# Optimization experiments

Hardware: AMD Instinct MI355X
Metric: run time of the kernel (lower is better)

Reference implementation:

```python
import jax, jax.numpy as jnp
import numpy as np

N = 10000        # num_nodes
E = 160000       # num_edges (before self loops)
D_IN = 256       # input_dim
H = 128          # hidden_dim (= per-head out_channels)
HEADS = 4
HD = HEADS * H   # 512
L = 16           # num_layers
OUT = 1024       # output_dim
G = 8            # num graphs in batch
EPS = 1e-5


def _layer_norm(x, w, b):
    m = jnp.mean(x, axis=-1, keepdims=True)
    v = jnp.mean(jnp.square(x - m), axis=-1, keepdims=True)
    return (x - m) / jnp.sqrt(v + EPS) * w + b


def setup_inputs() -> dict:
    key = jax.random.key(0)
    ks = jax.random.split(key, 20)
    s = 0.05
    x = jax.random.normal(ks[0], (N, D_IN), jnp.float32)
    edge_index = jax.random.randint(ks[1], (2, E), 0, N, dtype=jnp.int64)
    batch = jnp.sort(jax.random.randint(ks[2], (N,), 0, G, dtype=jnp.int64))
    return {
        "x": x,
        "edge_index": edge_index,
        "batch": batch,
        "W_in": jax.random.normal(ks[3], (D_IN, H), jnp.float32) * s,
        "b_in": jnp.zeros((H,), jnp.float32),
        "ln_in_w": jnp.ones((H,), jnp.float32),
        "ln_in_b": jnp.zeros((H,), jnp.float32),
        "Wsrc": jax.random.normal(ks[4], (L, H, HD), jnp.float32) * s,
        "Wdst": jax.random.normal(ks[5], (L, H, HD), jnp.float32) * s,
        "att_src": jax.random.normal(ks[6], (L, HEADS, H), jnp.float32) * s,
        "att_dst": jax.random.normal(ks[7], (L, HEADS, H), jnp.float32) * s,
        "Wout": jax.random.normal(ks[8], (L, HD, H), jnp.float32) * s,
        "bout": jnp.zeros((L, H), jnp.float32),
        "ln_w": jnp.ones((L, H), jnp.float32),
        "ln_b": jnp.zeros((L, H), jnp.float32),
        "Wp1": jax.random.normal(ks[9], (H, OUT), jnp.float32) * s,
        "bp1": jnp.zeros((OUT,), jnp.float32),
        "Wp2": jax.random.normal(ks[10], (OUT, OUT), jnp.float32) * s,
        "bp2": jnp.zeros((OUT,), jnp.float32),
    }


def reference(x, edge_index, batch, W_in, b_in, ln_in_w, ln_in_b,
              Wsrc, Wdst, att_src, att_dst, Wout, bout, ln_w, ln_b,
              Wp1, bp1, Wp2, bp2):
    # add self loops once (same edge set every layer)
    loop = jnp.arange(N, dtype=edge_index.dtype)
    e_src = jnp.concatenate([edge_index[0], loop])  # x_j (source)
    e_dst = jnp.concatenate([edge_index[1], loop])  # x_i (target / aggregate index)

    h = jax.nn.relu(_layer_norm(x @ W_in + b_in, ln_in_w, ln_in_b))  # [N, H]

    for l in range(L):
        hs = (h[e_src] @ Wsrc[l]).reshape(-1, HEADS, H)  # [E2, heads, H]
        hd = (h[e_dst] @ Wdst[l]).reshape(-1, HEADS, H)
        a = jnp.sum(hs * att_src[l], axis=-1) + jnp.sum(hd * att_dst[l], axis=-1)  # [E2, heads]
        a = jax.nn.leaky_relu(a, 0.2)
        # NOTE: faithful to source -- softmax over HEADS per edge, not over neighbors
        a = jax.nn.softmax(a, axis=-1)
        msg = (hs * a[..., None]).reshape(-1, HD)  # [E2, HD]
        agg = jax.ops.segment_sum(msg, e_dst, num_segments=N)  # [N, HD]
        out = agg @ Wout[l] + bout[l]
        h = jax.nn.relu(_layer_norm(out + h, ln_w[l], ln_b[l]))  # residual: H == H

    g = jax.ops.segment_max(h, batch, num_segments=G)  # global max pool [G, H]
    g = jax.nn.relu(g @ Wp1 + bp1)
    return g @ Wp2 + bp2  # [G, OUT]
```

## Files before the change

kernel.cpp:

```cpp
#include <hip/hip_runtime.h>
#include <hip/hip_bf16.h>

#define N_NODES 10000
#define E_EDGES 160000
#define E2 (E_EDGES + N_NODES)
#define D_IN 256
#define H 128
#define HEADS 4
#define HD 512
#define L_LAYERS 16
#define OUT_DIM 1024
#define G_GRAPHS 8
#define EPS 1e-5f
#define SPAD 10016

typedef unsigned short ushort_t;
typedef __attribute__((ext_vector_type(8))) short short8;
typedef __attribute__((ext_vector_type(4))) float f32x4;
typedef __attribute__((ext_vector_type(4))) unsigned u32x4;

__device__ __forceinline__ f32x4 mfma16(short8 a, short8 b, f32x4 c) {
    return __builtin_amdgcn_mfma_f32_16x16x32_bf16(a, b, c, 0, 0, 0);
}
__device__ __forceinline__ unsigned short f2b(float f) {
    unsigned u = __float_as_uint(f);
    u += 0x7fffu + ((u >> 16) & 1u);
    return (unsigned short)(u >> 16);
}
__device__ __forceinline__ float b2f(unsigned short b) {
    return __uint_as_float((unsigned)b << 16);
}
__device__ __forceinline__ unsigned pk2(float lo, float hi) {
    __hip_bfloat162 p = __float22bfloat162_rn(make_float2(lo, hi));
    return *(unsigned*)&p;
}

__global__ void k_zero(int* deg, int* cur, unsigned* g) {
    int i = blockIdx.x * blockDim.x + threadIdx.x;
    if (i < N_NODES) { deg[i] = 0; cur[i] = 0; }
    if (i < G_GRAPHS * H) g[i] = 0u;
}

__global__ void k_count(const int* ei, int* deg) {
    int e = blockIdx.x * blockDim.x + threadIdx.x;
    if (e >= E2) return;
    int d = (e < E_EDGES) ? ei[E_EDGES + e] : (e - E_EDGES);
    atomicAdd(&deg[d], 1);
}

__global__ void k_scan(const int* deg, int* rs) {
    __shared__ int s[1024];
    int t = threadIdx.x;
    int base = t * 10;
    int loc[10], run = 0;
    #pragma unroll
    for (int i = 0; i < 10; i++) {
        int idx = base + i;
        int v = (idx < N_NODES) ? deg[idx] : 0;
        loc[i] = run; run += v;
    }
    s[t] = run;
    __syncthreads();
    for (int off = 1; off < 1024; off <<= 1) {
        int xv = (t >= off) ? s[t - off] : 0;
        __syncthreads();
        s[t] += xv;
        __syncthreads();
    }
    int excl = s[t] - run;
    #pragma unroll
    for (int i = 0; i < 10; i++) {
        int idx = base + i;
        if (idx <= N_NODES) rs[idx] = excl + loc[i];
    }
}

__global__ void k_fill(const int* ei, const int* rs, int* cur, int* elist) {
    int e = blockIdx.x * blockDim.x + threadIdx.x;
    if (e >= E2) return;
    int s, d;
    if (e < E_EDGES) { s = ei[e]; d = ei[E_EDGES + e]; }
    else { s = d = e - E_EDGES; }
    int pos = atomicAdd(&cur[d], 1);
    elist[rs[d] + pos] = s;
}

__global__ void k_vw(const float* Wsrc, const float* Wdst,
                     const float* att_src, const float* att_dst,
                     float* vsrc, float* vdst) {
    int l = blockIdx.x;
    int t = threadIdx.x;
    int head = t >> 7, j = t & 127;
    const float* Ws = Wsrc + (size_t)l * H * HD;
    const float* Wd = Wdst + (size_t)l * H * HD;
    const float* As = att_src + (size_t)l * HEADS * H;
    const float* Ad = att_dst + (size_t)l * HEADS * H;
    float ss = 0.f, sd = 0.f;
    for (int k = 0; k < H; k++) {
        ss += Ws[(size_t)j * HD + head * H + k] * As[head * H + k];
        sd += Wd[(size_t)j * HD + head * H + k] * Ad[head * H + k];
    }
    vsrc[(size_t)l * HD + head * H + j] = ss;
    vdst[(size_t)l * HD + head * H + j] = sd;
}

__global__ __launch_bounds__(256) void k_mm(const float* __restrict__ Wsrc,
        const float* __restrict__ Wout, float* __restrict__ M) {
    __shared__ float As[32][33];
    __shared__ float Bs[32][128];
    int bid = blockIdx.x;
    int q = bid & 3, hh = (bid >> 2) & 3, l = bid >> 4;
    int t = threadIdx.x;
    int ty = t >> 4, tx = t & 15;
    const float* WsB = Wsrc + (size_t)l * H * HD + (size_t)hh * 128;
    const float* WoB = Wout + (size_t)l * HD * H + (size_t)hh * 128 * H;
    float acc[2][8];
    #pragma unroll
    for (int r = 0; r < 2; r++)
        #pragma unroll
        for (int c = 0; c < 8; c++) acc[r][c] = 0.f;
    for (int kt = 0; kt < 4; kt++) {
        #pragma unroll
        for (int i = 0; i < 4; i++) {
            int lin = i * 256 + t;
            int rr = lin >> 5, cc = lin & 31;
            As[rr][cc] = WsB[(size_t)(q * 32 + rr) * HD + kt * 32 + cc];
        }
        #pragma unroll
        for (int i = 0; i < 16; i++) {
            int lin = i * 256 + t;
            int rr = lin >> 7, cc = lin & 127;
            Bs[rr][cc] = WoB[(size_t)(kt * 32 + rr) * H + cc];
        }
        __syncthreads();
        #pragma unroll
        for (int kk = 0; kk < 32; kk++) {
            float a0 = As[ty * 2][kk], a1 = As[ty * 2 + 1][kk];
            float4 b0 = *(const float4*)&Bs[kk][tx * 8];
            float4 b1 = *(const float4*)&Bs[kk][tx * 8 + 4];
            acc[0][0] += a0 * b0.x; acc[0][1] += a0 * b0.y;
            acc[0][2] += a0 * b0.z; acc[0][3] += a0 * b0.w;
            acc[0][4] += a0 * b1.x; acc[0][5] += a0 * b1.y;
            acc[0][6] += a0 * b1.z; acc[0][7] += a0 * b1.w;
            acc[1][0] += a1 * b0.x; acc[1][1] += a1 * b0.y;
            acc[1][2] += a1 * b0.z; acc[1][3] += a1 * b0.w;
            acc[1][4] += a1 * b1.x; acc[1][5] += a1 * b1.y;
            acc[1][6] += a1 * b1.z; acc[1][7] += a1 * b1.w;
        }
        __syncthreads();
    }
    #pragma unroll
    for (int r = 0; r < 2; r++)
        #pragma unroll
        for (int c = 0; c < 8; c++)
            M[(size_t)l * HD * H + (size_t)(hh * 128 + q * 32 + ty * 2 + r) * H + tx * 8 + c]
                = acc[r][c];
}

__global__ void k_pack_out2(const float* M, ushort_t* Wh, ushort_t* Wl) {
    int idx = blockIdx.x * 256 + threadIdx.x;
    int l = idx >> 16, rem = idx & 65535;
    int k = rem >> 7, col = rem & 127;
    float v = M[(size_t)l * HD * H + (size_t)k * H + col];
    unsigned short hi = f2b(v);
    unsigned short lo = f2b(v - b2f(hi));
    int nt = col >> 4, ks = k >> 5, lhi = (k >> 3) & 3, llo = col & 15, j = k & 7;
    size_t addr = (size_t)l * 65536 + (((size_t)(nt * 16 + ks) * 64) + lhi * 16 + llo) * 8 + j;
    Wh[addr] = hi;
    Wl[addr] = lo;
}

__global__ void k_pack_win(const float* W, ushort_t* Wp) {
    int idx = blockIdx.x * 256 + threadIdx.x;
    int k = idx >> 7, col = idx & 127;
    float v = W[(size_t)k * H + col];
    int nt = col >> 4, ks = k >> 5, lhi = (k >> 3) & 3, llo = col & 15, j = k & 7;
    Wp[(((size_t)(nt * 8 + ks) * 64) + lhi * 16 + llo) * 8 + j] = f2b(v);
}

__global__ __launch_bounds__(256) void k_in_mfma(
        const float* __restrict__ x, const ushort_t* __restrict__ WpI,
        const float* __restrict__ b_in, const float* __restrict__ lnw,
        const float* __restrict__ lnb, const float* __restrict__ vs,
        const float* __restrict__ vd, float* __restrict__ as0, float* __restrict__ ad0,
        float* __restrict__ h, ushort_t* __restrict__ hb) {
    __shared__ float part1[4][16], part2[4][16];
    __shared__ float apart[4][8][16];
    int t = threadIdx.x, w = t >> 6, lane = t & 63;
    int row0 = blockIdx.x * 16;
    int ar = lane & 15, ac = (lane >> 4) * 8;
    short8 a[8];
    #pragma unroll
    for (int ks = 0; ks < 8; ks++) {
        const float* xp = x + (size_t)(row0 + ar) * D_IN + ks * 32 + ac;
        float4 xa = *(const float4*)xp;
        float4 xb = *(const float4*)(xp + 4);
        u32x4 u;
        u.x = pk2(xa.x, xa.y); u.y = pk2(xa.z, xa.w);
        u.z = pk2(xb.x, xb.y); u.w = pk2(xb.z, xb.w);
        a[ks] = *(short8*)&u;
    }
    const ushort_t* B0 = WpI + ((size_t)(w * 2 + 0) * 8) * 64 * 8;
    const ushort_t* B1 = WpI + ((size_t)(w * 2 + 1) * 8) * 64 * 8;
    f32x4 c0 = {0.f, 0.f, 0.f, 0.f}, c1 = {0.f, 0.f, 0.f, 0.f};
    #pragma unroll
    for (int ks = 0; ks < 8; ks++) {
        short8 b0 = *(const short8*)(B0 + ((size_t)ks * 64 + lane) * 8);
        short8 b1 = *(const short8*)(B1 + ((size_t)ks * 64 + lane) * 8);
        c0 = mfma16(a[ks], b0, c0);
        c1 = mfma16(a[ks], b1, c1);
    }
    int col0 = w * 32 + ar, col1 = w * 32 + 16 + ar;
    int rb = (lane >> 4) * 4;
    float v0[4], v1[4], y0[4], y1[4];
    #pragma unroll
    for (int r = 0; r < 4; r++) {
        v0[r] = c0[r] + b_in[col0];
        v1[r] = c1[r] + b_in[col1];
        float p1 = v0[r] + v1[r];
        float p2 = v0[r] * v0[r] + v1[r] * v1[r];
        #pragma unroll
        for (int off = 1; off < 16; off <<= 1) {
            p1 += __shfl_xor(p1, off);
            p2 += __shfl_xor(p2, off);
        }
        if (ar == 0) { part1[w][rb + r] = p1; part2[w][rb + r] = p2; }
    }
    __syncthreads();
    #pragma unroll
    for (int r = 0; r < 4; r++) {
        int lr = rb + r;
        int row = row0 + lr;
        float s1 = part1[0][lr] + part1[1][lr] + part1[2][lr] + part1[3][lr];
        float s2 = part2[0][lr] + part2[1][lr] + part2[2][lr] + part2[3][lr];
        float m = s1 * (1.f / 128.f);
        float var = s2 * (1.f / 128.f) - m * m;
        float is = rsqrtf(var + EPS);
        y0[r] = fmaxf((v0[r] - m) * is * lnw[col0] + lnb[col0], 0.f);
        y1[r] = fmaxf((v1[r] - m) * is * lnw[col1] + lnb[col1], 0.f);
        h[(size_t)row * H + col0] = y0[r];
        h[(size_t)row * H + col1] = y1[r];
        hb[(size_t)row * H + col0] = f2b(y0[r]);
        hb[(size_t)row * H + col1] = f2b(y1[r]);
    }
    #pragma unroll
    for (int comp = 0; comp < 8; comp++) {
        float vc0 = (comp < 4) ? vs[comp * H + col0] : vd[(comp - 4) * H + col0];
        float vc1 = (comp < 4) ? vs[comp * H + col1] : vd[(comp - 4) * H + col1];
        float p[4];
        #pragma unroll
        for (int r = 0; r < 4; r++) p[r] = y0[r] * vc0 + y1[r] * vc1;
        #pragma unroll
        for (int off = 1; off < 16; off <<= 1)
            #pragma unroll
            for (int r = 0; r < 4; r++) p[r] += __shfl_xor(p[r], off);
        if (ar == 0)
            #pragma unroll
            for (int r = 0; r < 4; r++) apart[w][comp][rb + r] = p[r];
    }
    __syncthreads();
    if (t < 128) {
        int lr = t >> 3, comp = t & 7;
        float s = apart[0][comp][lr] + apart[1][comp][lr]
                + apart[2][comp][lr] + apart[3][comp][lr];
        int node = row0 + lr;
        if (comp < 4) as0[node * 4 + comp] = s;
        else          ad0[node * 4 + comp - 4] = s;
    }
}

#define CONS(uv, wt) do { \
    float f0 = __uint_as_float((uv).x << 16); \
    float f1 = __uint_as_float((uv).x & 0xffff0000u); \
    float f2 = __uint_as_float((uv).y << 16); \
    float f3 = __uint_as_float((uv).y & 0xffff0000u); \
    float f4 = __uint_as_float((uv).z << 16); \
    float f5 = __uint_as_float((uv).z & 0xffff0000u); \
    float f6 = __uint_as_float((uv).w << 16); \
    float f7 = __uint_as_float((uv).w & 0xffff0000u); \
    acc0[0] += (wt).x * f0; acc0[1] += (wt).x * f1; acc0[2] += (wt).x * f2; acc0[3] += (wt).x * f3; \
    acc0[4] += (wt).x * f4; acc0[5] += (wt).x * f5; acc0[6] += (wt).x * f6; acc0[7] += (wt).x * f7; \
    acc1[0] += (wt).y * f0; acc1[1] += (wt).y * f1; acc1[2] += (wt).y * f2; acc1[3] += (wt).y * f3; \
    acc1[4] += (wt).y * f4; acc1[5] += (wt).y * f5; acc1[6] += (wt).y * f6; acc1[7] += (wt).y * f7; \
    acc2[0] += (wt).z * f0; acc2[1] += (wt).z * f1; acc2[2] += (wt).z * f2; acc2[3] += (wt).z * f3; \
    acc2[4] += (wt).z * f4; acc2[5] += (wt).z * f5; acc2[6] += (wt).z * f6; acc2[7] += (wt).z * f7; \
    acc3[0] += (wt).w * f0; acc3[1] += (wt).w * f1; acc3[2] += (wt).w * f2; acc3[3] += (wt).w * f3; \
    acc3[4] += (wt).w * f4; acc3[5] += (wt).w * f5; acc3[6] += (wt).w * f6; acc3[7] += (wt).w * f7; \
} while (0)

__global__ __launch_bounds__(256) void k_gather(
        const ushort_t* __restrict__ hb, const float4* __restrict__ as4,
        const float4* __restrict__ ad4, const int* __restrict__ rs,
        const int* __restrict__ elist, ushort_t* __restrict__ T) {
    __shared__ int sl[4][64];
    __shared__ float wl[4][64][4];
    int t = threadIdx.x, w = t >> 6, lane = t & 63;
    int node = blockIdx.x * 4 + w;
    int start = rs[node], end = rs[node + 1];
    int g = lane >> 4, i = lane & 15;
    const char* hbc = (const char*)hb;
    unsigned ibyte = (unsigned)(i << 4);
    float acc0[8], acc1[8], acc2[8], acc3[8];
    #pragma unroll
    for (int c = 0; c < 8; c++) { acc0[c] = 0.f; acc1[c] = 0.f; acc2[c] = 0.f; acc3[c] = 0.f; }
    for (int c0 = start; c0 < end; c0 += 64) {
        int cnt = min(64, end - c0);
        if (lane < cnt) {
            int s = elist[c0 + lane];
            sl[w][lane] = s;
            float4 adv = ad4[node];
            float4 av = as4[s];
            float l0 = av.x + adv.x, l1 = av.y + adv.y, l2 = av.z + adv.z, l3 = av.w + adv.w;
            l0 = (l0 > 0.f) ? l0 : 0.2f * l0;
            l1 = (l1 > 0.f) ? l1 : 0.2f * l1;
            l2 = (l2 > 0.f) ? l2 : 0.2f * l2;
            l3 = (l3 > 0.f) ? l3 : 0.2f * l3;
            float mx = fmaxf(fmaxf(l0, l1), fmaxf(l2, l3));
            float e0 = expf(l0 - mx), e1 = expf(l1 - mx), e2 = expf(l2 - mx), e3 = expf(l3 - mx);
            float inv = 1.f / (e0 + e1 + e2 + e3);
            wl[w][lane][0] = e0 * inv;
            wl[w][lane][1] = e1 * inv;
            wl[w][lane][2] = e2 * inv;
            wl[w][lane][3] = e3 * inv;
        } else {
            sl[w][lane] = 0;
            wl[w][lane][0] = 0.f; wl[w][lane][1] = 0.f;
            wl[w][lane][2] = 0.f; wl[w][lane][3] = 0.f;
        }
        __asm__ volatile("s_waitcnt lgkmcnt(0)" ::: "memory");
        int rounds = (cnt + 15) >> 4;
        for (int jj = 0; jj < rounds; jj++) {
            int j = (jj << 4) + g;
            unsigned o0 = ((unsigned)sl[w][j]      << 8) + ibyte;
            unsigned o1 = ((unsigned)sl[w][j + 4]  << 8) + ibyte;
            unsigned o2 = ((unsigned)sl[w][j + 8]  << 8) + ibyte;
            unsigned o3 = ((unsigned)sl[w][j + 12] << 8) + ibyte;
            u32x4 v0 = *(const u32x4*)(hbc + o0);
            u32x4 v1 = *(const u32x4*)(hbc + o1);
            u32x4 v2 = *(const u32x4*)(hbc + o2);
            u32x4 v3 = *(const u32x4*)(hbc + o3);
            { float4 wt = *(const float4*)wl[w][j];      CONS(v0, wt); }
            { float4 wt = *(const float4*)wl[w][j + 4];  CONS(v1, wt); }
            { float4 wt = *(const float4*)wl[w][j + 8];  CONS(v2, wt); }
            { float4 wt = *(const float4*)wl[w][j + 12]; CONS(v3, wt); }
        }
    }
    float out[8];
    #pragma unroll
    for (int c = 0; c < 8; c++) {
        float v0 = acc0[c], v1 = acc1[c], v2 = acc2[c], v3 = acc3[c];
        v0 += __shfl_xor(v0, 16); v0 += __shfl_xor(v0, 32);
        v1 += __shfl_xor(v1, 16); v1 += __shfl_xor(v1, 32);
        v2 += __shfl_xor(v2, 16); v2 += __shfl_xor(v2, 32);
        v3 += __shfl_xor(v3, 16); v3 += __shfl_xor(v3, 32);
        out[c] = (g == 0) ? v0 : ((g == 1) ? v1 : ((g == 2) ? v2 : v3));
    }
    u32x4 o;
    o.x = pk2(out[0], out[1]);
    o.y = pk2(out[2], out[3]);
    o.z = pk2(out[4], out[5]);
    o.w = pk2(out[6], out[7]);
    *(u32x4*)(T + (size_t)node * HD + g * 128 + i * 8) = o;
}

__global__ __launch_bounds__(256) void k_post(
        const ushort_t* __restrict__ T, const ushort_t* __restrict__ Wh,
        const ushort_t* __restrict__ Wl, const float* __restrict__ bout,
        const float* __restrict__ lnw, const float* __restrict__ lnb,
        const float* __restrict__ vsn, const float* __restrict__ vdn,
        float* __restrict__ asn, float* __restrict__ adn, int doAlpha,
        float* __restrict__ h, ushort_t* __restrict__ hbo, int l) {
    __shared__ ushort_t frag[1024 * 8];
    __shared__ float part1[4][16], part2[4][16];
    __shared__ float apart[4][8][16];
    int t = threadIdx.x, w = t >> 6, lane = t & 63;
    int row0 = blockIdx.x * 16;
    #pragma unroll
    for (int ii = 0; ii < 4; ii++) {
        int c = ii * 256 + t;
        int row = c >> 6, ks = (c >> 2) & 15, sub = c & 3;
        u32x4 v = *(const u32x4*)(T + (size_t)(row0 + row) * HD + ks * 32 + sub * 8);
        int gidx = (sub * 16 + row) * 16 + (ks ^ row);
        *(u32x4*)((char*)frag + gidx * 16) = v;
    }
    __syncthreads();
    int ar = lane & 15;
    short8 a[16];
    #pragma unroll
    for (int ks = 0; ks < 16; ks++)
        a[ks] = *(const short8*)((const char*)frag + (lane * 16 + (ks ^ ar)) * 16);
    const ushort_t* WLh = Wh + (size_t)l * 65536;
    const ushort_t* WLl = Wl + (size_t)l * 65536;
    f32x4 c0 = {0.f, 0.f, 0.f, 0.f}, c1 = {0.f, 0.f, 0.f, 0.f};
    #pragma unroll
    for (int ks = 0; ks < 16; ks++) {
        short8 b0 = *(const short8*)(WLh + ((size_t)((w * 2 + 0) * 16 + ks) * 64 + lane) * 8);
        short8 b1 = *(const short8*)(WLh + ((size_t)((w * 2 + 1) * 16 + ks) * 64 + lane) * 8);
        c0 = mfma16(a[ks], b0, c0);
        c1 = mfma16(a[ks], b1, c1);
    }
    #pragma unroll
    for (int ks = 0; ks < 16; ks++) {
        short8 b0 = *(const short8*)(WLl + ((size_t)((w * 2 + 0) * 16 + ks) * 64 + lane) * 8);
        short8 b1 = *(const short8*)(WLl + ((size_t)((w * 2 + 1) * 16 + ks) * 64 + lane) * 8);
        c0 = mfma16(a[ks], b0, c0);
        c1 = mfma16(a[ks], b1, c1);
    }
    const float* bo = bout + (size_t)l * H;
    const float* gw = lnw + (size_t)l * H;
    const float* gb = lnb + (size_t)l * H;
    int col0 = w * 32 + ar, col1 = w * 32 + 16 + ar;
    int rb = (lane >> 4) * 4;
    float v0[4], v1[4], y0[4], y1[4];
    #pragma unroll
    for (int r = 0; r < 4; r++) {
        int row = row0 + rb + r;
        v0[r] = c0[r] + bo[col0] + h[(size_t)row * H + col0];
        v1[r] = c1[r] + bo[col1] + h[(size_t)row * H + col1];
        float p1 = v0[r] + v1[r];
        float p2 = v0[r] * v0[r] + v1[r] * v1[r];
        #pragma unroll
        for (int off = 1; off < 16; off <<= 1) {
            p1 += __shfl_xor(p1, off);
            p2 += __shfl_xor(p2, off);
        }
        if (ar == 0) { part1[w][rb + r] = p1; part2[w][rb + r] = p2; }
    }
    __syncthreads();
    #pragma unroll
    for (int r = 0; r < 4; r++) {
        int lr = rb + r;
        int row = row0 + lr;
        float s1 = part1[0][lr] + part1[1][lr] + part1[2][lr] + part1[3][lr];
        float s2 = part2[0][lr] + part2[1][lr] + part2[2][lr] + part2[3][lr];
        float m = s1 * (1.f / 128.f);
        float var = s2 * (1.f / 128.f) - m * m;
        float is = rsqrtf(var + EPS);
        y0[r] = fmaxf((v0[r] - m) * is * gw[col0] + gb[col0], 0.f);
        y1[r] = fmaxf((v1[r] - m) * is * gw[col1] + gb[col1], 0.f);
        h[(size_t)row * H + col0] = y0[r];
        h[(size_t)row * H + col1] = y1[r];
        hbo[(size_t)row * H + col0] = f2b(y0[r]);
        hbo[(size_t)row * H + col1] = f2b(y1[r]);
    }
    if (doAlpha) {
        #pragma unroll
        for (int comp = 0; comp < 8; comp++) {
            float vc0 = (comp < 4) ? vsn[comp * H + col0] : vdn[(comp - 4) * H + col0];
            float vc1 = (comp < 4) ? vsn[comp * H + col1] : vdn[(comp - 4) * H + col1];
            float p[4];
            #pragma unroll
            for (int r = 0; r < 4; r++) p[r] = y0[r] * vc0 + y1[r] * vc1;
            #pragma unroll
            for (int off = 1; off < 16; off <<= 1)
                #pragma unroll
                for (int r = 0; r < 4; r++) p[r] += __shfl_xor(p[r], off);
            if (ar == 0)
                #pragma unroll
                for (int r = 0; r < 4; r++) apart[w][comp][rb + r] = p[r];
        }
        __syncthreads();
        if (t < 128) {
            int lr = t >> 3, comp = t & 7;
            float s = apart[0][comp][lr] + apart[1][comp][lr]
                    + apart[2][comp][lr] + apart[3][comp][lr];
            int node = row0 + lr;
            if (comp < 4) asn[node * 4 + comp] = s;
            else          adn[node * 4 + comp - 4] = s;
        }
    }
}

__global__ void k_pool(const float* __restrict__ h, const int* __restrict__ batch,
                       unsigned* __restrict__ g) {
    __shared__ float lm[G_GRAPHS][H];
    int t = threadIdx.x;
    #pragma unroll
    for (int i = 0; i < G_GRAPHS; i++) lm[i][t] = 0.f;
    int n0 = blockIdx.x * 100, n1 = n0 + 100;
    for (int n = n0; n < n1; n++) {
        int b = batch[n];
        lm[b][t] = fmaxf(lm[b][t], h[(size_t)n * H + t]);
    }
    #pragma unroll
    for (int i = 0; i < G_GRAPHS; i++)
        atomicMax(&g[i * H + t], __float_as_uint(lm[i][t]));
}

__global__ void k_mlp1(const unsigned* __restrict__ g, const float* __restrict__ Wp1,
                       const float* __restrict__ bp1, float* __restrict__ g1) {
    __shared__ float gs[H];
    int gr = blockIdx.x >> 2, ch = blockIdx.x & 3;
    int t = threadIdx.x;
    if (t < H) gs[t] = __uint_as_float(g[gr * H + t]);
    __syncthreads();
    int col = ch * 256 + t;
    float acc = 0.f;
    for (int k = 0; k < H; k++) acc += gs[k] * Wp1[(size_t)k * OUT_DIM + col];
    acc += bp1[col];
    g1[(size_t)gr * OUT_DIM + col] = fmaxf(acc, 0.f);
}

__global__ void k_mlp2(const float* __restrict__ g1, const float* __restrict__ Wp2,
                       const float* __restrict__ bp2, float* __restrict__ out) {
    __shared__ float gs[OUT_DIM];
    __shared__ float part[4][64];
    int gr = blockIdx.x >> 4, ch = blockIdx.x & 15;
    int t = threadIdx.x;
    int ci = t & 63, si = t >> 6;
    for (int i = t; i < OUT_DIM; i += 256) gs[i] = g1[(size_t)gr * OUT_DIM + i];
    __syncthreads();
    int col = ch * 64 + ci;
    float acc = 0.f;
    for (int k = si * 256; k < si * 256 + 256; k++)
        acc += gs[k] * Wp2[(size_t)k * OUT_DIM + col];
    part[si][ci] = acc;
    __syncthreads();
    if (si == 0) {
        float r = part[0][ci] + part[1][ci] + part[2][ci] + part[3][ci] + bp2[col];
        out[(size_t)gr * OUT_DIM + col] = r;
    }
}

extern "C" void kernel_launch(void* const* d_in, const int* in_sizes, int n_in,
                              void* d_out, int out_size, void* d_ws, size_t ws_size,
                              hipStream_t stream) {
    const float* x       = (const float*)d_in[0];
    const int*   ei      = (const int*)d_in[1];
    const int*   batch   = (const int*)d_in[2];
    const float* W_in    = (const float*)d_in[3];
    const float* b_in    = (const float*)d_in[4];
    const float* ln_in_w = (const float*)d_in[5];
    const float* ln_in_b = (const float*)d_in[6];
    const float* Wsrc    = (const float*)d_in[7];
    const float* Wdst    = (const float*)d_in[8];
    const float* att_src = (const float*)d_in[9];
    const float* att_dst = (const float*)d_in[10];
    const float* Wout    = (const float*)d_in[11];
    const float* bout    = (const float*)d_in[12];
    const float* ln_w    = (const float*)d_in[13];
    const float* ln_b    = (const float*)d_in[14];
    const float* Wp1     = (const float*)d_in[15];
    const float* bp1     = (const float*)d_in[16];
    const float* Wp2     = (const float*)d_in[17];
    const float* bp2     = (const float*)d_in[18];

    char* w = (char*)d_ws;
    auto alloc = [&](size_t bytes) { void* p = w; w += (bytes + 255) & ~(size_t)255; return p; };
    float*     h     = (float*)alloc((size_t)N_NODES * H * 4);
    ushort_t*  hb0   = (ushort_t*)alloc((size_t)SPAD * H * 2);
    ushort_t*  hb1   = (ushort_t*)alloc((size_t)SPAD * H * 2);
    ushort_t*  T     = (ushort_t*)alloc((size_t)SPAD * HD * 2);
    float*     as0   = (float*)alloc((size_t)SPAD * HEADS * 4);
    float*     ad0   = (float*)alloc((size_t)SPAD * HEADS * 4);
    float*     as1   = (float*)alloc((size_t)SPAD * HEADS * 4);
    float*     ad1   = (float*)alloc((size_t)SPAD * HEADS * 4);
    float*     vsrc  = (float*)alloc((size_t)L_LAYERS * HD * 4);
    float*     vdst  = (float*)alloc((size_t)L_LAYERS * HD * 4);
    float*     M     = (float*)alloc((size_t)L_LAYERS * HD * H * 4);
    ushort_t*  WpH   = (ushort_t*)alloc((size_t)L_LAYERS * 65536 * 2);
    ushort_t*  WpL   = (ushort_t*)alloc((size_t)L_LAYERS * 65536 * 2);
    ushort_t*  WpI   = (ushort_t*)alloc((size_t)D_IN * H * 2);
    int*       deg   = (int*)alloc((size_t)N_NODES * 4);
    int*       rs    = (int*)alloc((size_t)(N_NODES + 1) * 4);
    int*       cur   = (int*)alloc((size_t)N_NODES * 4);
    int*       elist = (int*)alloc((size_t)E2 * 4);
    unsigned*  g     = (unsigned*)alloc((size_t)G_GRAPHS * H * 4);
    float*     g1    = (float*)alloc((size_t)G_GRAPHS * OUT_DIM * 4);

    k_zero<<<40, 256, 0, stream>>>(deg, cur, g);
    k_count<<<(E2 + 255) / 256, 256, 0, stream>>>(ei, deg);
    k_scan<<<1, 1024, 0, stream>>>(deg, rs);
    k_fill<<<(E2 + 255) / 256, 256, 0, stream>>>(ei, rs, cur, elist);
    k_vw<<<L_LAYERS, 512, 0, stream>>>(Wsrc, Wdst, att_src, att_dst, vsrc, vdst);
    k_mm<<<256, 256, 0, stream>>>(Wsrc, Wout, M);
    k_pack_out2<<<4096, 256, 0, stream>>>(M, WpH, WpL);
    k_pack_win<<<128, 256, 0, stream>>>(W_in, WpI);
    k_in_mfma<<<N_NODES / 16, 256, 0, stream>>>(x, WpI, b_in, ln_in_w, ln_in_b,
                                                vsrc, vdst, as0, ad0, h, hb0);

    for (int l = 0; l < L_LAYERS; l++) {
        const ushort_t* hbi = (l & 1) ? hb1 : hb0;
        ushort_t*       hbo = (l & 1) ? hb0 : hb1;
        const float* aA = (l & 1) ? as1 : as0;
        const float* dA = (l & 1) ? ad1 : ad0;
        float* aB = (l & 1) ? as0 : as1;
        float* dB = (l & 1) ? ad0 : ad1;
        int ln = (l + 1 < L_LAYERS) ? (l + 1) : (L_LAYERS - 1);
        k_gather<<<N_NODES / 4, 256, 0, stream>>>(hbi, (const float4*)aA, (const float4*)dA,
                                                  rs, elist, T);
        k_post<<<N_NODES / 16, 256, 0, stream>>>(
            T, WpH, WpL, bout, ln_w, ln_b,
            vsrc + (size_t)ln * HD, vdst + (size_t)ln * HD,
            aB, dB, (l + 1 < L_LAYERS) ? 1 : 0, h, hbo, l);
    }

    k_pool<<<100, 128, 0, stream>>>(h, batch, g);
    k_mlp1<<<G_GRAPHS * 4, 256, 0, stream>>>(g, Wp1, bp1, g1);
    k_mlp2<<<G_GRAPHS * 16, 256, 0, stream>>>(g1, Wp2, bp2, (float*)d_out);
}
```

Before: 728.6 us.

## Parallelize attention-vector precompute, add nontemporal hints, trim gather tail loop

The per-layer attention-vector kernel is rewritten so that each wavefront reduces one output with a shuffle reduction, replacing the old layout of 16 blocks with a serial 128-step loop per thread and strided loads. Streaming buffers (h, the T intermediate) now use nontemporal loads and stores so they bypass cache retention. The gather loop now processes neighbors in 4-wide steps for the remainder instead of padding to a multiple of 16. Nontemporal hints could hurt if these buffers benefit from L2/MALL reuse between kernels.

```diff
diff --git a/kernel.cpp b/kernel.cpp
--- a/kernel.cpp
+++ b/kernel.cpp
@@ -85,23 +85,29 @@
     elist[rs[d] + pos] = s;
 }
 
-__global__ void k_vw(const float* Wsrc, const float* Wdst,
-                     const float* att_src, const float* att_dst,
-                     float* vsrc, float* vdst) {
-    int l = blockIdx.x;
-    int t = threadIdx.x;
-    int head = t >> 7, j = t & 127;
-    const float* Ws = Wsrc + (size_t)l * H * HD;
-    const float* Wd = Wdst + (size_t)l * H * HD;
-    const float* As = att_src + (size_t)l * HEADS * H;
-    const float* Ad = att_dst + (size_t)l * HEADS * H;
-    float ss = 0.f, sd = 0.f;
-    for (int k = 0; k < H; k++) {
-        ss += Ws[(size_t)j * HD + head * H + k] * As[head * H + k];
-        sd += Wd[(size_t)j * HD + head * H + k] * Ad[head * H + k];
-    }
-    vsrc[(size_t)l * HD + head * H + j] = ss;
-    vdst[(size_t)l * HD + head * H + j] = sd;
+__global__ __launch_bounds__(256) void k_vw(const float* __restrict__ Wsrc,
+        const float* __restrict__ Wdst, const float* __restrict__ att_src,
+        const float* __restrict__ att_dst, float* __restrict__ vsrc,
+        float* __restrict__ vdst) {
+    int t = threadIdx.x, w = t >> 6, lane = t & 63;
+    int unit = blockIdx.x * 4 + w;
+    int j = unit & 127, head = (unit >> 7) & 3, l = unit >> 9;
+    int k2 = lane * 2;
+    const float2 ws = *(const float2*)(Wsrc + (size_t)l * H * HD + (size_t)j * HD + head * 128 + k2);
+    const float2 wd = *(const float2*)(Wdst + (size_t)l * H * HD + (size_t)j * HD + head * 128 + k2);
+    const float2 as = *(const float2*)(att_src + (size_t)l * HEADS * H + head * 128 + k2);
+    const float2 ad = *(const float2*)(att_dst + (size_t)l * HEADS * H + head * 128 + k2);
+    float p = ws.x * as.x + ws.y * as.y;
+    float q = wd.x * ad.x + wd.y * ad.y;
+    #pragma unroll
+    for (int off = 32; off > 0; off >>= 1) {
+        p += __shfl_down(p, off);
+        q += __shfl_down(q, off);
+    }
+    if (lane == 0) {
+        vsrc[(size_t)l * HD + head * H + j] = p;
+        vdst[(size_t)l * HD + head * H + j] = q;
+    }
 }
 
 __global__ __launch_bounds__(256) void k_mm(const float* __restrict__ Wsrc,
@@ -238,8 +244,8 @@
         float is = rsqrtf(var + EPS);
         y0[r] = fmaxf((v0[r] - m) * is * lnw[col0] + lnb[col0], 0.f);
         y1[r] = fmaxf((v1[r] - m) * is * lnw[col1] + lnb[col1], 0.f);
-        h[(size_t)row * H + col0] = y0[r];
-        h[(size_t)row * H + col1] = y1[r];
+        __builtin_nontemporal_store(y0[r], &h[(size_t)row * H + col0]);
+        __builtin_nontemporal_store(y1[r], &h[(size_t)row * H + col1]);
         hb[(size_t)row * H + col0] = f2b(y0[r]);
         hb[(size_t)row * H + col1] = f2b(y1[r]);
     }
@@ -328,8 +334,8 @@
             wl[w][lane][2] = 0.f; wl[w][lane][3] = 0.f;
         }
         __asm__ volatile("s_waitcnt lgkmcnt(0)" ::: "memory");
-        int rounds = (cnt + 15) >> 4;
-        for (int jj = 0; jj < rounds; jj++) {
+        int full = cnt >> 4;
+        for (int jj = 0; jj < full; jj++) {
             int j = (jj << 4) + g;
             unsigned o0 = ((unsigned)sl[w][j]      << 8) + ibyte;
             unsigned o1 = ((unsigned)sl[w][j + 4]  << 8) + ibyte;
@@ -344,6 +350,13 @@
             { float4 wt = *(const float4*)wl[w][j + 8];  CONS(v2, wt); }
             { float4 wt = *(const float4*)wl[w][j + 12]; CONS(v3, wt); }
         }
+        for (int j0 = full << 4; j0 < cnt; j0 += 4) {
+            int j = j0 + g;
+            unsigned o0 = ((unsigned)sl[w][j] << 8) + ibyte;
+            u32x4 v0 = *(const u32x4*)(hbc + o0);
+            float4 wt = *(const float4*)wl[w][j];
+            CONS(v0, wt);
+        }
     }
     float out[8];
     #pragma unroll
@@ -360,7 +373,7 @@
     o.y = pk2(out[2], out[3]);
     o.z = pk2(out[4], out[5]);
     o.w = pk2(out[6], out[7]);
-    *(u32x4*)(T + (size_t)node * HD + g * 128 + i * 8) = o;
+    __builtin_nontemporal_store(o, (u32x4*)(T + (size_t)node * HD + g * 128 + i * 8));
 }
 
 __global__ __launch_bounds__(256) void k_post(
@@ -379,7 +392,8 @@
     for (int ii = 0; ii < 4; ii++) {
         int c = ii * 256 + t;
         int row = c >> 6, ks = (c >> 2) & 15, sub = c & 3;
-        u32x4 v = *(const u32x4*)(T + (size_t)(row0 + row) * HD + ks * 32 + sub * 8);
+        u32x4 v = __builtin_nontemporal_load(
+            (const u32x4*)(T + (size_t)(row0 + row) * HD + ks * 32 + sub * 8));
         int gidx = (sub * 16 + row) * 16 + (ks ^ row);
         *(u32x4*)((char*)frag + gidx * 16) = v;
     }
@@ -415,8 +429,8 @@
     #pragma unroll
     for (int r = 0; r < 4; r++) {
         int row = row0 + rb + r;
-        v0[r] = c0[r] + bo[col0] + h[(size_t)row * H + col0];
-        v1[r] = c1[r] + bo[col1] + h[(size_t)row * H + col1];
+        v0[r] = c0[r] + bo[col0] + __builtin_nontemporal_load(&h[(size_t)row * H + col0]);
+        v1[r] = c1[r] + bo[col1] + __builtin_nontemporal_load(&h[(size_t)row * H + col1]);
         float p1 = v0[r] + v1[r];
         float p2 = v0[r] * v0[r] + v1[r] * v1[r];
         #pragma unroll
@@ -438,8 +452,8 @@
         float is = rsqrtf(var + EPS);
         y0[r] = fmaxf((v0[r] - m) * is * gw[col0] + gb[col0], 0.f);
         y1[r] = fmaxf((v1[r] - m) * is * gw[col1] + gb[col1], 0.f);
-        h[(size_t)row * H + col0] = y0[r];
-        h[(size_t)row * H + col1] = y1[r];
+        __builtin_nontemporal_store(y0[r], &h[(size_t)row * H + col0]);
+        __builtin_nontemporal_store(y1[r], &h[(size_t)row * H + col1]);
         hbo[(size_t)row * H + col0] = f2b(y0[r]);
         hbo[(size_t)row * H + col1] = f2b(y1[r]);
     }
@@ -572,7 +586,7 @@
     k_count<<<(E2 + 255) / 256, 256, 0, stream>>>(ei, deg);
     k_scan<<<1, 1024, 0, stream>>>(deg, rs);
     k_fill<<<(E2 + 255) / 256, 256, 0, stream>>>(ei, rs, cur, elist);
-    k_vw<<<L_LAYERS, 512, 0, stream>>>(Wsrc, Wdst, att_src, att_dst, vsrc, vdst);
+    k_vw<<<2048, 256, 0, stream>>>(Wsrc, Wdst, att_src, att_dst, vsrc, vdst);
     k_mm<<<256, 256, 0, stream>>>(Wsrc, Wout, M);
     k_pack_out2<<<4096, 256, 0, stream>>>(M, WpH, WpL);
     k_pack_win<<<128, 256, 0, stream>>>(W_in, WpI);
```

Result: no change. 714.4 us (-2.0%).
